# Optimization experiments

Hardware: AMD Instinct MI355X
Metric: run time of the kernel (lower is better)

Reference implementation:

```python
import jax, jax.numpy as jnp
import numpy as np

N = 131072
L_ENC = 100
L_DEC = 50
H = 200            # decoder_hidden_dim
SPD = L_ENC + 2 * (L_ENC // 2 + 1)  # 202, signal + amplitudes + phases


def _lin(k, out_d, in_d):
    kw, kb = jax.random.split(k)
    lim = 1.0 / np.sqrt(in_d)
    w = jax.random.uniform(kw, (out_d, in_d), jnp.float32, -lim, lim)
    b = jax.random.uniform(kb, (out_d,), jnp.float32, -lim, lim)
    return w, b


def setup_inputs() -> dict:
    key = jax.random.key(0)
    ks = jax.random.split(key, 16)
    enc_w1, enc_b1 = _lin(ks[0], 100, SPD)
    enc_w2, enc_b2 = _lin(ks[1], SPD, 100)
    enc_wl, enc_bl = _lin(ks[2], H, SPD)
    lim = 1.0 / np.sqrt(H)
    w_ih = jax.random.uniform(ks[3], (3 * H, 1), jnp.float32, -lim, lim)
    w_hh = jax.random.uniform(ks[4], (3 * H, H), jnp.float32, -lim, lim)
    b_ih = jax.random.uniform(ks[5], (3 * H,), jnp.float32, -lim, lim)
    b_hh = jax.random.uniform(ks[6], (3 * H,), jnp.float32, -lim, lim)
    dec_w1, dec_b1 = _lin(ks[7], H // 2, H)
    dec_w2, dec_b2 = _lin(ks[8], H // 4, H // 2)
    dec_w3, dec_b3 = _lin(ks[9], 1, H // 4)
    encoder_input = jax.random.normal(ks[10], (N, L_ENC, 1), jnp.float32)
    return dict(encoder_input=encoder_input,
                enc_w1=enc_w1, enc_b1=enc_b1, enc_w2=enc_w2, enc_b2=enc_b2,
                enc_wl=enc_wl, enc_bl=enc_bl,
                w_ih=w_ih, w_hh=w_hh, b_ih=b_ih, b_hh=b_hh,
                dec_w1=dec_w1, dec_b1=dec_b1, dec_w2=dec_w2, dec_b2=dec_b2,
                dec_w3=dec_w3, dec_b3=dec_b3)


def _lrelu(x):
    return jax.nn.leaky_relu(x, negative_slope=0.01)


def reference(encoder_input, enc_w1, enc_b1, enc_w2, enc_b2, enc_wl, enc_bl,
              w_ih, w_hh, b_ih, b_hh,
              dec_w1, dec_b1, dec_w2, dec_b2, dec_w3, dec_b3):
    # --- MLPEncoder: rfft features + 3-layer MLP ---
    f = jnp.fft.rfft(encoder_input, axis=1, norm='forward')  # [N, 51, 1] complex
    sig = jnp.concatenate([encoder_input, jnp.abs(f), jnp.angle(f)], axis=1)[..., 0]  # [N, 202]
    x = _lrelu(sig @ enc_w1.T + enc_b1)
    x = _lrelu(x @ enc_w2.T + enc_b2)
    h0 = x @ enc_wl.T + enc_bl  # [N, H]

    dec_in0 = encoder_input[:, -1, :]  # [N, 1]

    def step(carry, _):
        h, dec_in = carry
        gx = dec_in @ w_ih.T + b_ih       # [N, 3H]
        gh = h @ w_hh.T + b_hh            # [N, 3H]
        xr, xz, xn = jnp.split(gx, 3, axis=-1)
        hr, hz, hn = jnp.split(gh, 3, axis=-1)
        r = jax.nn.sigmoid(xr + hr)
        z = jax.nn.sigmoid(xz + hz)
        n = jnp.tanh(xn + r * hn)
        h_new = (1.0 - z) * n + z * h
        y = _lrelu(h_new @ dec_w1.T + dec_b1)
        y = _lrelu(y @ dec_w2.T + dec_b2)
        y = y @ dec_w3.T + dec_b3         # [N, 1]
        return (h_new, jax.lax.stop_gradient(y)), y

    _, ys = jax.lax.scan(step, (h0, dec_in0), None, length=L_DEC)  # [L_DEC, N, 1]
    return jnp.transpose(ys, (1, 0, 2))  # [N, L_DEC, 1]
```

## Files before the change

### kernel.cpp

```cpp
#include <hip/hip_runtime.h>
#include <math.h>

typedef _Float16 half8  __attribute__((ext_vector_type(8)));
typedef float    floatx4 __attribute__((ext_vector_type(4)));

#define MFMA16(a, b, c) __builtin_amdgcn_mfma_f32_16x16x32_f16((a), (b), (c), 0, 0, 0)

constexpr unsigned WBIG_OFF = 0;
constexpr unsigned W2_OFF   = 329728;
constexpr unsigned WE1_OFF  = 346112;
constexpr unsigned WE2_OFF  = 396288;
constexpr unsigned WEL_OFF  = 449536;
constexpr unsigned WIHC_OFF = 542720;
constexpr unsigned BSUM_OFF = 545216;
constexpr unsigned BHHN_OFF = 547712;
constexpr unsigned B1P_OFF  = 548544;
constexpr unsigned B2P_OFF  = 548992;
constexpr unsigned W3P_OFF  = 549248;
constexpr unsigned BE1_OFF  = 549504;
constexpr unsigned BE2_OFF  = 549952;
constexpr unsigned BEL_OFF  = 550784;
constexpr unsigned B3_OFF   = 551616;
constexpr unsigned CT_OFF   = 551632;
constexpr unsigned WS_NEED  = 553232;

constexpr unsigned BST_OFF   = 106496;
constexpr unsigned W2L_OFF   = 128000;
constexpr unsigned CHK_OFF   = 145408;
constexpr unsigned DECIN_OFF = 161792;
constexpr unsigned SMEM_BYTES = 162816;

__device__ __forceinline__ half8 lds_frag16(const _Float16* p) {
  union { uint4 u; half8 h; } cv;
  cv.u = *(const uint4*)p;
  return cv.h;
}
__device__ __forceinline__ half8 g_frag(const _Float16* p) {
  union { uint4 u; half8 h; } cv;
  cv.u = *(const uint4*)p;
  return cv.h;
}
__device__ __forceinline__ void gload_lds16(const _Float16* gsrc, _Float16* lds) {
  __builtin_amdgcn_global_load_lds(
      (const __attribute__((address_space(1))) unsigned int*)gsrc,
      (__attribute__((address_space(3))) unsigned int*)lds, 16, 0, 0);
}
__device__ __forceinline__ float sigm(float x) {
  return __builtin_amdgcn_rcpf(1.f + __builtin_amdgcn_exp2f(-1.44269504f * x));
}
__device__ __forceinline__ float tanh_(float x) {
  return 1.f - 2.f * __builtin_amdgcn_rcpf(1.f + __builtin_amdgcn_exp2f(2.88539008f * x));
}

__global__ __launch_bounds__(256) void prep_kernel(
    const float* __restrict__ enc_w1, const float* __restrict__ enc_b1,
    const float* __restrict__ enc_w2, const float* __restrict__ enc_b2,
    const float* __restrict__ enc_wl, const float* __restrict__ enc_bl,
    const float* __restrict__ w_ih,  const float* __restrict__ w_hh,
    const float* __restrict__ b_ih,  const float* __restrict__ b_hh,
    const float* __restrict__ dw1, const float* __restrict__ db1,
    const float* __restrict__ dw2, const float* __restrict__ db2,
    const float* __restrict__ dw3, const float* __restrict__ db3,
    unsigned char* __restrict__ ws)
{
  const int g = blockIdx.x * blockDim.x + threadIdx.x;
  const int st = gridDim.x * blockDim.x;
  _Float16* Wbig = (_Float16*)(ws + WBIG_OFF);
  for (int i = g; i < 736 * 224; i += st) {
    int row = i / 224, k = i - row * 224;
    float v = 0.f;
    if (k < 200) {
      if (row < 624) { int gg = row / 208, j = row - gg * 208;
        if (j < 200) v = w_hh[(gg * 200 + j) * 200 + k]; }
      else { int j = row - 624; if (j < 100) v = dw1[j * 200 + k]; }
    }
    Wbig[i] = (_Float16)v;
  }
  _Float16* W2 = (_Float16*)(ws + W2_OFF);
  for (int i = g; i < 64 * 128; i += st) {
    int r = i / 128, k = i - r * 128;
    W2[i] = (_Float16)((r < 50 && k < 100) ? dw2[r * 100 + k] : 0.f);
  }
  _Float16* We1 = (_Float16*)(ws + WE1_OFF);
  for (int i = g; i < 112 * 224; i += st) {
    int r = i / 224, k = i - r * 224;
    We1[i] = (_Float16)((r < 100 && k < 202) ? enc_w1[r * 202 + k] : 0.f);
  }
  _Float16* We2 = (_Float16*)(ws + WE2_OFF);
  for (int i = g; i < 208 * 128; i += st) {
    int r = i / 128, k = i - r * 128;
    We2[i] = (_Float16)((r < 202 && k < 100) ? enc_w2[r * 100 + k] : 0.f);
  }
  _Float16* Wel = (_Float16*)(ws + WEL_OFF);
  for (int i = g; i < 208 * 224; i += st) {
    int r = i / 224, k = i - r * 224;
    Wel[i] = (_Float16)((r < 200 && k < 202) ? enc_wl[r * 202 + k] : 0.f);
  }
  float* wihc = (float*)(ws + WIHC_OFF);
  float* bsum = (float*)(ws + BSUM_OFF);
  for (int i = g; i < 624; i += st) {
    int gg = i / 208, j = i - gg * 208;
    wihc[i] = (j < 200) ? w_ih[gg * 200 + j] : 0.f;
    float b = 0.f;
    if (j < 200) b = (gg < 2) ? (b_ih[gg * 200 + j] + b_hh[gg * 200 + j]) : b_ih[400 + j];
    bsum[i] = b;
  }
  float* bhhn = (float*)(ws + BHHN_OFF);
  for (int i = g; i < 208; i += st) bhhn[i] = (i < 200) ? b_hh[400 + i] : 0.f;
  float* b1p = (float*)(ws + B1P_OFF);
  for (int i = g; i < 112; i += st) b1p[i] = (i < 100) ? db1[i] : 0.f;
  float* b2p = (float*)(ws + B2P_OFF);
  for (int i = g; i < 64; i += st) b2p[i] = (i < 50) ? db2[i] : 0.f;
  float* w3p = (float*)(ws + W3P_OFF);
  for (int i = g; i < 64; i += st) w3p[i] = (i < 50) ? dw3[i] : 0.f;
  float* be1 = (float*)(ws + BE1_OFF);
  for (int i = g; i < 112; i += st) be1[i] = (i < 100) ? enc_b1[i] : 0.f;
  float* be2 = (float*)(ws + BE2_OFF);
  for (int i = g; i < 208; i += st) be2[i] = (i < 202) ? enc_b2[i] : 0.f;
  float* bel = (float*)(ws + BEL_OFF);
  for (int i = g; i < 208; i += st) bel[i] = (i < 200) ? enc_bl[i] : 0.f;
  if (g == 0) *(float*)(ws + B3_OFF) = db3[0];
  double* ct = (double*)(ws + CT_OFF);
  for (int m = g; m < 100; m += st) {
    double c, s;
    if      (m == 0)  { c = 1.0;  s = 0.0; }
    else if (m == 25) { c = 0.0;  s = -1.0; }
    else if (m == 50) { c = -1.0; s = 0.0; }
    else if (m == 75) { c = 0.0;  s = 1.0; }
    else { double a = -2.0 * 3.14159265358979323846 * (double)m / 100.0; c = cos(a); s = sin(a); }
    ct[2 * m]     = c * 0.01;
    ct[2 * m + 1] = s * 0.01;
  }
}

__global__ __launch_bounds__(512, 1) void fused_kernel(
    const float* __restrict__ enc_in, const unsigned char* __restrict__ ws,
    float* __restrict__ out)
{
  __shared__ __align__(16) unsigned char smem[SMEM_BYTES];
  _Float16* Hb    = (_Float16*)smem;
  _Float16* BST   = (_Float16*)(smem + BST_OFF);
  _Float16* W2L   = (_Float16*)(smem + W2L_OFF);
  float*    DECIN = (float*)(smem + DECIN_OFF);
  double*   CTL   = (double*)(smem + CHK_OFF);

  const _Float16* Wbig = (const _Float16*)(ws + WBIG_OFF);
  const _Float16* W2w  = (const _Float16*)(ws + W2_OFF);
  const _Float16* We1  = (const _Float16*)(ws + WE1_OFF);
  const _Float16* We2  = (const _Float16*)(ws + WE2_OFF);
  const _Float16* Wel  = (const _Float16*)(ws + WEL_OFF);
  const float* wihc = (const float*)(ws + WIHC_OFF);
  const float* bsum = (const float*)(ws + BSUM_OFF);
  const float* bhhn = (const float*)(ws + BHHN_OFF);
  const float* b1p  = (const float*)(ws + B1P_OFF);
  const float* b2p  = (const float*)(ws + B2P_OFF);
  const float* w3p  = (const float*)(ws + W3P_OFF);
  const float* be1  = (const float*)(ws + BE1_OFF);
  const float* be2  = (const float*)(ws + BE2_OFF);
  const float* bel  = (const float*)(ws + BEL_OFF);
  const float b3v   = *(const float*)(ws + B3_OFF);

  const int tid = threadIdx.x;
  const int lane = tid & 63, wv = tid >> 6;
  const int q = lane >> 4, c = lane & 15;
  const int row0 = blockIdx.x * 256;
  const half8 Z8 = {};

  {
    const double* ctg = (const double*)(ws + CT_OFF);
    for (int i = tid; i < 200; i += 512) CTL[i] = ctg[i];
  }

#pragma unroll 1
  for (int sub = 0; sub < 4; ++sub) {
    float*    XF  = (float*)(smem + sub * 26624);
    _Float16* X1  = (_Float16*)(smem + sub * 26624);
    _Float16* SIG = (_Float16*)(smem + BST_OFF);
    __syncthreads();
    for (int i = tid; i < 6400; i += 512) {
      int r = i / 100, t = i - r * 100;
      XF[r * 101 + t] = enc_in[(size_t)(row0 + sub * 64 + r) * 100 + t];
    }
    for (int i = tid; i < 64 * 6; i += 512) {
      int r = i / 6; SIG[r * 208 + 202 + (i - r * 6)] = (_Float16)0.f;
    }
    __syncthreads();
    for (int kb = wv; kb < 51; kb += 8) {
      double re = 0.0, im = 0.0; int m = 0;
      const float* xr = XF + lane * 101;
      for (int t = 0; t < 100; ++t) {
        double x = (double)xr[t];
        re = fma(x, CTL[2 * m], re);
        im = fma(x, CTL[2 * m + 1], im);
        m += kb; if (m >= 100) m -= 100;
      }
      if (kb == 0 || kb == 50) im = 0.0;
      float ab = (float)sqrt(re * re + im * im);
      float an = atan2f((float)im, (float)re);
      SIG[lane * 208 + 100 + kb] = (_Float16)ab;
      SIG[lane * 208 + 151 + kb] = (_Float16)an;
    }
    for (int i = tid; i < 6400; i += 512) {
      int r = i / 100, t = i - r * 100;
      SIG[r * 208 + t] = (_Float16)XF[r * 101 + t];
    }
    __syncthreads();
#pragma unroll 1
    for (int jt = wv; jt < 7; jt += 8) {
      floatx4 C[4] = {{0,0,0,0},{0,0,0,0},{0,0,0,0},{0,0,0,0}};
      const _Float16* wp = We1 + (jt * 16 + c) * 224 + q * 8;
#pragma unroll
      for (int s = 0; s < 7; ++s) {
        half8 B = g_frag(wp + s * 32);
#pragma unroll
        for (int m = 0; m < 4; ++m) {
          half8 Af = (s == 6 && q >= 2) ? Z8 : lds_frag16(SIG + (m * 16 + c) * 208 + q * 8 + s * 32);
          C[m] = MFMA16(Af, B, C[m]);
        }
      }
      int col = jt * 16 + c; float bv = be1[col]; bool wm = col < 104;
#pragma unroll
      for (int m = 0; m < 4; ++m)
#pragma unroll
        for (int r = 0; r < 4; ++r) {
          float v = C[m][r] + bv; v = fmaxf(v, 0.01f * v);
          if (wm) X1[(m * 16 + 4 * q + r) * 104 + col] = (_Float16)v;
        }
    }
    __syncthreads();
#pragma unroll 1
    for (int jt = wv; jt < 13; jt += 8) {
      floatx4 C[4] = {{0,0,0,0},{0,0,0,0},{0,0,0,0},{0,0,0,0}};
      const _Float16* wp = We2 + (jt * 16 + c) * 128 + q * 8;
#pragma unroll
      for (int s = 0; s < 4; ++s) {
        half8 B = g_frag(wp + s * 32);
#pragma unroll
        for (int m = 0; m < 4; ++m) {
          half8 Af = (s == 3 && q >= 1) ? Z8 : lds_frag16(X1 + (m * 16 + c) * 104 + q * 8 + s * 32);
          C[m] = MFMA16(Af, B, C[m]);
        }
      }
      int col = jt * 16 + c; float bv = be2[col];
#pragma unroll
      for (int m = 0; m < 4; ++m)
#pragma unroll
        for (int r = 0; r < 4; ++r) {
          float v = C[m][r] + bv; v = fmaxf(v, 0.01f * v);
          SIG[(m * 16 + 4 * q + r) * 208 + col] = (_Float16)v;
        }
    }
    __syncthreads();
#pragma unroll 1
    for (int jt = wv; jt < 13; jt += 8) {
      floatx4 C[4] = {{0,0,0,0},{0,0,0,0},{0,0,0,0},{0,0,0,0}};
      const _Float16* wp = Wel + (jt * 16 + c) * 224 + q * 8;
#pragma unroll
      for (int s = 0; s < 7; ++s) {
        half8 B = g_frag(wp + s * 32);
#pragma unroll
        for (int m = 0; m < 4; ++m) {
          half8 Af = (s == 6 && q >= 2) ? Z8 : lds_frag16(SIG + (m * 16 + c) * 208 + q * 8 + s * 32);
          C[m] = MFMA16(Af, B, C[m]);
        }
      }
      int col = jt * 16 + c; float bv = bel[col]; bool wm = col < 200;
#pragma unroll
      for (int m = 0; m < 4; ++m)
#pragma unroll
        for (int r = 0; r < 4; ++r) {
          float v = C[m][r] + bv;
          if (wm) Hb[(sub * 64 + m * 16 + 4 * q + r) * 208 + col] = (_Float16)v;
        }
    }
  }
  __syncthreads();
  for (int i = tid; i < 256 * 8; i += 512) {
    int r = i / 8; Hb[r * 208 + 200 + (i - r * 8)] = (_Float16)0.f;
  }
  for (int i = tid; i < 256; i += 512)
    DECIN[i] = enc_in[(size_t)(row0 + i) * 100 + 99];
  for (int i = tid; i < 1024; i += 512) {
    int r = i / 16, kc = i - r * 16;
    *(uint4*)(W2L + r * 136 + kc * 8) = *(const uint4*)(W2w + r * 128 + kc * 8);
  }
  __syncthreads();

  _Float16* myH   = Hb + wv * 32 * 208;
  _Float16* myCHK = (_Float16*)(smem + CHK_OFF) + wv * 1024;

#pragma unroll 1
  for (int k = 0; k <= 50; ++k) {
    half8 A[2][7];
#pragma unroll
    for (int m = 0; m < 2; ++m)
#pragma unroll
      for (int s = 0; s < 7; ++s)
        A[m][s] = (s == 6 && q >= 2) ? Z8 : lds_frag16(myH + (m * 16 + c) * 208 + s * 32 + q * 8);

    if (k >= 1) {
      half8 A2[2][4];
#pragma unroll
      for (int jtp = 0; jtp < 4; ++jtp) {
        const int njt = (jtp == 3) ? 1 : 2;
        __syncthreads();
        for (int i = wv; i < njt * 7; i += 8) {
          int jj = i / 7, p = i - jj * 7;
          gload_lds16(Wbig + (624 + (jtp * 2 + jj) * 16) * 224 + p * 512 + lane * 8,
                      BST + jj * 3584 + p * 512);
        }
        __syncthreads();
#pragma unroll
        for (int jj = 0; jj < 2; ++jj) {
          if (jj < njt) {
            floatx4 C[2] = {{0,0,0,0},{0,0,0,0}};
#pragma unroll
            for (int s = 0; s < 7; ++s) {
              half8 B = lds_frag16(BST + jj * 3584 + c * 224 + s * 32 + q * 8);
#pragma unroll
              for (int m = 0; m < 2; ++m) C[m] = MFMA16(A[m][s], B, C[m]);
            }
            int col = (jtp * 2 + jj) * 16 + c; float bv = b1p[col];
#pragma unroll
            for (int m = 0; m < 2; ++m)
#pragma unroll
              for (int r = 0; r < 4; ++r) {
                float v = C[m][r] + bv; v = fmaxf(v, 0.01f * v);
                myCHK[(m * 16 + 4 * q + r) * 32 + jj * 16 + c] = (_Float16)v;
              }
          }
        }
#pragma unroll
        for (int m = 0; m < 2; ++m)
          A2[m][jtp] = (jtp == 3 && q >= 2) ? Z8 : lds_frag16(myCHK + (m * 16 + c) * 32 + q * 8);
      }
      float ya[2][4] = {{0,0,0,0},{0,0,0,0}};
#pragma unroll
      for (int jt2 = 0; jt2 < 4; ++jt2) {
        floatx4 Cy[2] = {{0,0,0,0},{0,0,0,0}};
#pragma unroll
        for (int s2 = 0; s2 < 4; ++s2) {
          half8 B = lds_frag16(W2L + (jt2 * 16 + c) * 136 + s2 * 32 + q * 8);
#pragma unroll
          for (int m = 0; m < 2; ++m) Cy[m] = MFMA16(A2[m][s2], B, Cy[m]);
        }
        int col2 = jt2 * 16 + c; float b2v = b2p[col2], w3v = w3p[col2];
#pragma unroll
        for (int m = 0; m < 2; ++m)
#pragma unroll
          for (int r = 0; r < 4; ++r) {
            float v = Cy[m][r] + b2v; v = fmaxf(v, 0.01f * v);
            ya[m][r] = fmaf(v, w3v, ya[m][r]);
          }
      }
#pragma unroll
      for (int m = 0; m < 2; ++m)
#pragma unroll
        for (int r = 0; r < 4; ++r) {
          float v = ya[m][r];
          v += __shfl_xor(v, 1); v += __shfl_xor(v, 2);
          v += __shfl_xor(v, 4); v += __shfl_xor(v, 8);
          if (c == 0) {
            int rowL = wv * 32 + m * 16 + 4 * q + r;
            float y = v + b3v;
            DECIN[rowL] = y;
            out[(size_t)(row0 + rowL) * 50 + (k - 1)] = y;
          }
        }
    }
    if (k <= 49) {
      float dreg[8];
#pragma unroll
      for (int m = 0; m < 2; ++m)
#pragma unroll
        for (int r = 0; r < 4; ++r)
          dreg[m * 4 + r] = DECIN[wv * 32 + m * 16 + 4 * q + r];
#pragma unroll 1
      for (int jt = 0; jt < 13; ++jt) {
        __syncthreads();
        for (int i = wv; i < 21; i += 8) {
          int g = i / 7, p = i - g * 7;
          gload_lds16(Wbig + (g * 208 + jt * 16) * 224 + p * 512 + lane * 8,
                      BST + g * 3584 + p * 512);
        }
        __syncthreads();
        floatx4 Cr[2] = {{0,0,0,0},{0,0,0,0}};
        floatx4 Cz[2] = {{0,0,0,0},{0,0,0,0}};
        floatx4 Cn[2] = {{0,0,0,0},{0,0,0,0}};
#pragma unroll
        for (int s = 0; s < 7; ++s) {
          half8 Br = lds_frag16(BST + c * 224 + s * 32 + q * 8);
          half8 Bz = lds_frag16(BST + 3584 + c * 224 + s * 32 + q * 8);
          half8 Bn = lds_frag16(BST + 7168 + c * 224 + s * 32 + q * 8);
#pragma unroll
          for (int m = 0; m < 2; ++m) {
            Cr[m] = MFMA16(A[m][s], Br, Cr[m]);
            Cz[m] = MFMA16(A[m][s], Bz, Cz[m]);
            Cn[m] = MFMA16(A[m][s], Bn, Cn[m]);
          }
        }
        int col = jt * 16 + c;
        float wr = wihc[col], wz = wihc[208 + col], wn = wihc[416 + col];
        float br = bsum[col], bz = bsum[208 + col], bnih = bsum[416 + col];
        float bnhh = bhhn[col];
        bool wm = col < 200;
#pragma unroll
        for (int m = 0; m < 2; ++m) {
          _Float16* hp = myH + (m * 16 + 4 * q) * 208 + col;
#pragma unroll
          for (int r = 0; r < 4; ++r) {
            float d  = dreg[m * 4 + r];
            float ho = (float)hp[r * 208];
            float rgate = sigm(Cr[m][r] + fmaf(d, wr, br));
            float zgate = sigm(Cz[m][r] + fmaf(d, wz, bz));
            float ngate = tanh_(fmaf(d, wn, bnih) + rgate * (Cn[m][r] + bnhh));
            float hv = fmaf(zgate, ho - ngate, ngate);
            if (wm) hp[r * 208] = (_Float16)hv;
          }
        }
      }
    }
  }
}

extern "C" void kernel_launch(void* const* d_in, const int* in_sizes, int n_in,
                              void* d_out, int out_size, void* d_ws, size_t ws_size,
                              hipStream_t stream) {
  const float* enc_in = (const float*)d_in[0];
  const float* enc_w1 = (const float*)d_in[1];
  const float* enc_b1 = (const float*)d_in[2];
  const float* enc_w2 = (const float*)d_in[3];
  const float* enc_b2 = (const float*)d_in[4];
  const float* enc_wl = (const float*)d_in[5];
  const float* enc_bl = (const float*)d_in[6];
  const float* w_ih   = (const float*)d_in[7];
  const float* w_hh   = (const float*)d_in[8];
  const float* b_ih   = (const float*)d_in[9];
  const float* b_hh   = (const float*)d_in[10];
  const float* dw1    = (const float*)d_in[11];
  const float* db1    = (const float*)d_in[12];
  const float* dw2    = (const float*)d_in[13];
  const float* db2    = (const float*)d_in[14];
  const float* dw3    = (const float*)d_in[15];
  const float* db3    = (const float*)d_in[16];
  unsigned char* ws = (unsigned char*)d_ws;
  float* out = (float*)d_out;

  prep_kernel<<<dim3(256), dim3(256), 0, stream>>>(
      enc_w1, enc_b1, enc_w2, enc_b2, enc_wl, enc_bl,
      w_ih, w_hh, b_ih, b_hh, dw1, db1, dw2, db2, dw3, db3, ws);
  fused_kernel<<<dim3(512), dim3(512), 0, stream>>>(enc_in, ws, out);
}
```

Baseline: 3.608 ms.

## Double-buffer GRU weight tiles in LDS with fragment-major prepacked layout

The prep kernel now stores the GRU hidden weights and the decoder dw1/dw2 weights pre-arranged in MFMA fragment order, so each lane fetches a contiguous 16-byte chunk. The GRU step ping-pongs between two LDS buffers, loading tile jt+1 while tile jt is computed, which drops one of the two barriers per tile. The decoder MLP now reads its B fragments straight from global memory instead of staging them in LDS. The hidden-state stride shrinks from 208 to 200 with an XOR swizzle on the scratch chunk. In exchange, the A fragments for the padded K columns now read neighbouring data, which is only harmless because those weights are zero-filled, and the decoder now depends on global or L2 latency.

```diff
diff --git a/kernel.cpp b/kernel.cpp
--- a/kernel.cpp
+++ b/kernel.cpp
@@ -6,8 +6,9 @@
 
 #define MFMA16(a, b, c) __builtin_amdgcn_mfma_f32_16x16x32_f16((a), (b), (c), 0, 0, 0)
 
-constexpr unsigned WBIG_OFF = 0;
-constexpr unsigned W2_OFF   = 329728;
+constexpr unsigned WJT_OFF  = 0;
+constexpr unsigned WD1_OFF  = 279552;
+constexpr unsigned W2F_OFF  = 329728;
 constexpr unsigned WE1_OFF  = 346112;
 constexpr unsigned WE2_OFF  = 396288;
 constexpr unsigned WEL_OFF  = 449536;
@@ -22,12 +23,12 @@
 constexpr unsigned BEL_OFF  = 550784;
 constexpr unsigned B3_OFF   = 551616;
 constexpr unsigned CT_OFF   = 551632;
-constexpr unsigned WS_NEED  = 553232;
-
-constexpr unsigned BST_OFF   = 106496;
-constexpr unsigned W2L_OFF   = 128000;
+
+constexpr unsigned GB0_OFF   = 102400;
+constexpr unsigned GB1_OFF   = 123904;
 constexpr unsigned CHK_OFF   = 145408;
 constexpr unsigned DECIN_OFF = 161792;
+constexpr unsigned CTL_OFF   = 129024;
 constexpr unsigned SMEM_BYTES = 162816;
 
 __device__ __forceinline__ half8 lds_frag16(const _Float16* p) {
@@ -50,6 +51,9 @@
 }
 __device__ __forceinline__ float tanh_(float x) {
   return 1.f - 2.f * __builtin_amdgcn_rcpf(1.f + __builtin_amdgcn_exp2f(2.88539008f * x));
+}
+__device__ __forceinline__ int chk_idx(int row, int col) {
+  return (row * 32 + col) ^ (((row >> 1) & 3) << 3);
 }
 
 __global__ __launch_bounds__(256) void prep_kernel(
@@ -65,21 +69,33 @@
 {
   const int g = blockIdx.x * blockDim.x + threadIdx.x;
   const int st = gridDim.x * blockDim.x;
-  _Float16* Wbig = (_Float16*)(ws + WBIG_OFF);
-  for (int i = g; i < 736 * 224; i += st) {
-    int row = i / 224, k = i - row * 224;
-    float v = 0.f;
-    if (k < 200) {
-      if (row < 624) { int gg = row / 208, j = row - gg * 208;
-        if (j < 200) v = w_hh[(gg * 200 + j) * 200 + k]; }
-      else { int j = row - 624; if (j < 100) v = dw1[j * 200 + k]; }
-    }
-    Wbig[i] = (_Float16)v;
-  }
-  _Float16* W2 = (_Float16*)(ws + W2_OFF);
-  for (int i = g; i < 64 * 128; i += st) {
-    int r = i / 128, k = i - r * 128;
-    W2[i] = (_Float16)((r < 50 && k < 100) ? dw2[r * 100 + k] : 0.f);
+  _Float16* WJT = (_Float16*)(ws + WJT_OFF);
+  for (int i = g; i < 13 * 10752; i += st) {
+    int jt = i / 10752, r1 = i - jt * 10752;
+    int gg = r1 / 3584,  r2 = r1 - gg * 3584;
+    int s  = r2 / 512,   r3 = r2 - s * 512;
+    int ln = r3 >> 3, j = r3 & 7;
+    int col = jt * 16 + (ln & 15);
+    int kk  = s * 32 + (ln >> 4) * 8 + j;
+    WJT[i] = (_Float16)((col < 200 && kk < 200) ? w_hh[(gg * 200 + col) * 200 + kk] : 0.f);
+  }
+  _Float16* WD1 = (_Float16*)(ws + WD1_OFF);
+  for (int i = g; i < 7 * 3584; i += st) {
+    int t = i / 3584, r1 = i - t * 3584;
+    int s = r1 / 512, r3 = r1 - s * 512;
+    int ln = r3 >> 3, j = r3 & 7;
+    int col = t * 16 + (ln & 15);
+    int kk  = s * 32 + (ln >> 4) * 8 + j;
+    WD1[i] = (_Float16)((col < 100 && kk < 200) ? dw1[col * 200 + kk] : 0.f);
+  }
+  _Float16* W2F = (_Float16*)(ws + W2F_OFF);
+  for (int i = g; i < 4 * 2048; i += st) {
+    int j2 = i / 2048, r1 = i - j2 * 2048;
+    int s2 = r1 / 512, r3 = r1 - s2 * 512;
+    int ln = r3 >> 3, j = r3 & 7;
+    int col = j2 * 16 + (ln & 15);
+    int kk  = s2 * 32 + (ln >> 4) * 8 + j;
+    W2F[i] = (_Float16)((col < 50 && kk < 100) ? dw2[col * 100 + kk] : 0.f);
   }
   _Float16* We1 = (_Float16*)(ws + WE1_OFF);
   for (int i = g; i < 112 * 224; i += st) {
@@ -139,13 +155,14 @@
 {
   __shared__ __align__(16) unsigned char smem[SMEM_BYTES];
   _Float16* Hb    = (_Float16*)smem;
-  _Float16* BST   = (_Float16*)(smem + BST_OFF);
-  _Float16* W2L   = (_Float16*)(smem + W2L_OFF);
+  _Float16* GB0   = (_Float16*)(smem + GB0_OFF);
+  _Float16* GB1   = (_Float16*)(smem + GB1_OFF);
   float*    DECIN = (float*)(smem + DECIN_OFF);
-  double*   CTL   = (double*)(smem + CHK_OFF);
-
-  const _Float16* Wbig = (const _Float16*)(ws + WBIG_OFF);
-  const _Float16* W2w  = (const _Float16*)(ws + W2_OFF);
+  double*   CTL   = (double*)(smem + CTL_OFF);
+
+  const _Float16* WJTp = (const _Float16*)(ws + WJT_OFF);
+  const _Float16* WD1f = (const _Float16*)(ws + WD1_OFF);
+  const _Float16* W2f  = (const _Float16*)(ws + W2F_OFF);
   const _Float16* We1  = (const _Float16*)(ws + WE1_OFF);
   const _Float16* We2  = (const _Float16*)(ws + WE2_OFF);
   const _Float16* Wel  = (const _Float16*)(ws + WEL_OFF);
@@ -163,6 +180,7 @@
   const int tid = threadIdx.x;
   const int lane = tid & 63, wv = tid >> 6;
   const int q = lane >> 4, c = lane & 15;
+  const int lf = lane * 8;
   const int row0 = blockIdx.x * 256;
   const half8 Z8 = {};
 
@@ -173,13 +191,13 @@
 
 #pragma unroll 1
   for (int sub = 0; sub < 4; ++sub) {
-    float*    XF  = (float*)(smem + sub * 26624);
-    _Float16* X1  = (_Float16*)(smem + sub * 26624);
-    _Float16* SIG = (_Float16*)(smem + BST_OFF);
+    float*    XF  = (float*)(smem + sub * 25600);
+    _Float16* X1  = (_Float16*)(smem + sub * 25600);
+    _Float16* SIG = (_Float16*)(smem + GB0_OFF);
     __syncthreads();
     for (int i = tid; i < 6400; i += 512) {
       int r = i / 100, t = i - r * 100;
-      XF[r * 101 + t] = enc_in[(size_t)(row0 + sub * 64 + r) * 100 + t];
+      XF[r * 100 + t] = enc_in[(size_t)(row0 + sub * 64 + r) * 100 + t];
     }
     for (int i = tid; i < 64 * 6; i += 512) {
       int r = i / 6; SIG[r * 208 + 202 + (i - r * 6)] = (_Float16)0.f;
@@ -187,7 +205,7 @@
     __syncthreads();
     for (int kb = wv; kb < 51; kb += 8) {
       double re = 0.0, im = 0.0; int m = 0;
-      const float* xr = XF + lane * 101;
+      const float* xr = XF + lane * 100;
       for (int t = 0; t < 100; ++t) {
         double x = (double)xr[t];
         re = fma(x, CTL[2 * m], re);
@@ -202,7 +220,7 @@
     }
     for (int i = tid; i < 6400; i += 512) {
       int r = i / 100, t = i - r * 100;
-      SIG[r * 208 + t] = (_Float16)XF[r * 101 + t];
+      SIG[r * 208 + t] = (_Float16)XF[r * 100 + t];
     }
     __syncthreads();
 #pragma unroll 1
@@ -270,23 +288,14 @@
 #pragma unroll
         for (int r = 0; r < 4; ++r) {
           float v = C[m][r] + bv;
-          if (wm) Hb[(sub * 64 + m * 16 + 4 * q + r) * 208 + col] = (_Float16)v;
-        }
-    }
-  }
-  __syncthreads();
-  for (int i = tid; i < 256 * 8; i += 512) {
-    int r = i / 8; Hb[r * 208 + 200 + (i - r * 8)] = (_Float16)0.f;
+          if (wm) Hb[(sub * 64 + m * 16 + 4 * q + r) * 200 + col] = (_Float16)v;
+        }
+    }
   }
   for (int i = tid; i < 256; i += 512)
     DECIN[i] = enc_in[(size_t)(row0 + i) * 100 + 99];
-  for (int i = tid; i < 1024; i += 512) {
-    int r = i / 16, kc = i - r * 16;
-    *(uint4*)(W2L + r * 136 + kc * 8) = *(const uint4*)(W2w + r * 128 + kc * 8);
-  }
   __syncthreads();
 
-  _Float16* myH   = Hb + wv * 32 * 208;
   _Float16* myCHK = (_Float16*)(smem + CHK_OFF) + wv * 1024;
 
 #pragma unroll 1
@@ -296,43 +305,42 @@
     for (int m = 0; m < 2; ++m)
 #pragma unroll
       for (int s = 0; s < 7; ++s)
-        A[m][s] = (s == 6 && q >= 2) ? Z8 : lds_frag16(myH + (m * 16 + c) * 208 + s * 32 + q * 8);
+        A[m][s] = lds_frag16(Hb + (wv * 32 + m * 16 + c) * 200 + s * 32 + q * 8);
+
+    __syncthreads();
+    if (k <= 49)
+      for (int i = wv; i < 21; i += 8)
+        gload_lds16(WJTp + i * 512 + lf, GB0 + i * 512);
 
     if (k >= 1) {
       half8 A2[2][4];
 #pragma unroll
-      for (int jtp = 0; jtp < 4; ++jtp) {
-        const int njt = (jtp == 3) ? 1 : 2;
-        __syncthreads();
-        for (int i = wv; i < njt * 7; i += 8) {
-          int jj = i / 7, p = i - jj * 7;
-          gload_lds16(Wbig + (624 + (jtp * 2 + jj) * 16) * 224 + p * 512 + lane * 8,
-                      BST + jj * 3584 + p * 512);
-        }
-        __syncthreads();
-#pragma unroll
-        for (int jj = 0; jj < 2; ++jj) {
-          if (jj < njt) {
-            floatx4 C[2] = {{0,0,0,0},{0,0,0,0}};
-#pragma unroll
-            for (int s = 0; s < 7; ++s) {
-              half8 B = lds_frag16(BST + jj * 3584 + c * 224 + s * 32 + q * 8);
-#pragma unroll
-              for (int m = 0; m < 2; ++m) C[m] = MFMA16(A[m][s], B, C[m]);
-            }
-            int col = (jtp * 2 + jj) * 16 + c; float bv = b1p[col];
-#pragma unroll
-            for (int m = 0; m < 2; ++m)
-#pragma unroll
-              for (int r = 0; r < 4; ++r) {
-                float v = C[m][r] + bv; v = fmaxf(v, 0.01f * v);
-                myCHK[(m * 16 + 4 * q + r) * 32 + jj * 16 + c] = (_Float16)v;
-              }
+      for (int t = 0; t < 7; ++t) {
+        floatx4 C[2] = {{0,0,0,0},{0,0,0,0}};
+#pragma unroll
+        for (int s = 0; s < 7; ++s) {
+          half8 B = g_frag(WD1f + (t * 7 + s) * 512 + lf);
+#pragma unroll
+          for (int m = 0; m < 2; ++m) C[m] = MFMA16(A[m][s], B, C[m]);
+        }
+        int col = t * 16 + c; float bv = b1p[col];
+#pragma unroll
+        for (int m = 0; m < 2; ++m)
+#pragma unroll
+          for (int r = 0; r < 4; ++r) {
+            float v = C[m][r] + bv; v = fmaxf(v, 0.01f * v);
+            myCHK[chk_idx(m * 16 + 4 * q + r, (t & 1) * 16 + c)] = (_Float16)v;
           }
-        }
-#pragma unroll
-        for (int m = 0; m < 2; ++m)
-          A2[m][jtp] = (jtp == 3 && q >= 2) ? Z8 : lds_frag16(myCHK + (m * 16 + c) * 32 + q * 8);
+        if (t & 1) {
+#pragma unroll
+          for (int m = 0; m < 2; ++m)
+            A2[m][t >> 1] = lds_frag16(myCHK + chk_idx(m * 16 + c, q * 8));
+        }
+        if (t == 6) {
+#pragma unroll
+          for (int m = 0; m < 2; ++m)
+            A2[m][3] = lds_frag16(myCHK + chk_idx(m * 16 + c, q * 8));
+        }
       }
       float ya[2][4] = {{0,0,0,0},{0,0,0,0}};
 #pragma unroll
@@ -340,7 +348,7 @@
         floatx4 Cy[2] = {{0,0,0,0},{0,0,0,0}};
 #pragma unroll
         for (int s2 = 0; s2 < 4; ++s2) {
-          half8 B = lds_frag16(W2L + (jt2 * 16 + c) * 136 + s2 * 32 + q * 8);
+          half8 B = g_frag(W2f + (jt2 * 4 + s2) * 512 + lf);
 #pragma unroll
           for (int m = 0; m < 2; ++m) Cy[m] = MFMA16(A2[m][s2], B, Cy[m]);
         }
@@ -378,20 +386,21 @@
 #pragma unroll 1
       for (int jt = 0; jt < 13; ++jt) {
         __syncthreads();
-        for (int i = wv; i < 21; i += 8) {
-          int g = i / 7, p = i - g * 7;
-          gload_lds16(Wbig + (g * 208 + jt * 16) * 224 + p * 512 + lane * 8,
-                      BST + g * 3584 + p * 512);
-        }
-        __syncthreads();
+        if (jt < 12) {
+          _Float16* dst = ((jt + 1) & 1) ? GB1 : GB0;
+          const _Float16* src = WJTp + (jt + 1) * 10752;
+          for (int i = wv; i < 21; i += 8)
+            gload_lds16(src + i * 512 + lf, dst + i * 512);
+        }
+        const _Float16* buf = (jt & 1) ? GB1 : GB0;
         floatx4 Cr[2] = {{0,0,0,0},{0,0,0,0}};
         floatx4 Cz[2] = {{0,0,0,0},{0,0,0,0}};
         floatx4 Cn[2] = {{0,0,0,0},{0,0,0,0}};
 #pragma unroll
         for (int s = 0; s < 7; ++s) {
-          half8 Br = lds_frag16(BST + c * 224 + s * 32 + q * 8);
-          half8 Bz = lds_frag16(BST + 3584 + c * 224 + s * 32 + q * 8);
-          half8 Bn = lds_frag16(BST + 7168 + c * 224 + s * 32 + q * 8);
+          half8 Br = lds_frag16(buf + s * 512 + lf);
+          half8 Bz = lds_frag16(buf + (7 + s) * 512 + lf);
+          half8 Bn = lds_frag16(buf + (14 + s) * 512 + lf);
 #pragma unroll
           for (int m = 0; m < 2; ++m) {
             Cr[m] = MFMA16(A[m][s], Br, Cr[m]);
@@ -406,16 +415,16 @@
         bool wm = col < 200;
 #pragma unroll
         for (int m = 0; m < 2; ++m) {
-          _Float16* hp = myH + (m * 16 + 4 * q) * 208 + col;
+          _Float16* hp = Hb + (wv * 32 + m * 16 + 4 * q) * 200 + col;
 #pragma unroll
           for (int r = 0; r < 4; ++r) {
             float d  = dreg[m * 4 + r];
-            float ho = (float)hp[r * 208];
+            float ho = (float)hp[r * 200];
             float rgate = sigm(Cr[m][r] + fmaf(d, wr, br));
             float zgate = sigm(Cz[m][r] + fmaf(d, wz, bz));
             float ngate = tanh_(fmaf(d, wn, bnih) + rgate * (Cn[m][r] + bnhh));
             float hv = fmaf(zgate, ho - ngate, ngate);
-            if (wm) hp[r * 208] = (_Float16)hv;
+            if (wm) hp[r * 200] = (_Float16)hv;
           }
         }
       }
```

Result: slower. 5.408 ms (+49.9%).
